# Kernel tuning notes

Hardware: AMD Instinct MI355X
Metric: run time of the kernel (lower is better)

Reference implementation:

```python
import jax, jax.numpy as jnp
import numpy as np

NBINS = 256  # tf.histogram_fixed_width(..., nbins=256)


def _colorspace():
    # tf.clip_by_value(tf.range(-1.0, 1.01, delta=1/127), -1, 1) -> 256 values
    cs = -1.0 + jnp.arange(NBINS, dtype=jnp.float32) / 127.0
    return jnp.clip(cs, -1.0, 1.0)


def _equalize_histogram(chan):
    # chan: (H, W) float32 in [-1, 1]
    h, w = chan.shape
    v = jnp.clip(chan.ravel(), -1.0, 1.0)
    idx = jnp.clip(((v + 1.0) * (NBINS / 2.0)).astype(jnp.int32), 0, NBINS - 1)
    hist = jnp.zeros(NBINS, jnp.int32).at[idx].add(1)
    cdf = jnp.cumsum(hist)
    cdf_min = jnp.min(cdf)
    pix_cnt = float(h * w)
    return (cdf - cdf_min).astype(jnp.float32) * 2.0 / (pix_cnt - 1.0) - 1.0


def _interpolate(dx, dy, x):
    # dx, dy: (K,) ; x: (N,) -> (N,) piecewise-linear interp via nearest-bin argmin
    delvals = jnp.abs(dx[None, :] - x[:, None])  # (N, K) big intermediate, as in TF
    ind1 = jnp.argmin(delvals, axis=1)
    ind0 = jnp.maximum(ind1 - 1, 0)
    x0, x1 = dx[ind0], dx[ind1]
    y0, y1 = dy[ind0], dy[ind1]
    denom = x1 - x0
    safe = jnp.where(denom == 0.0, 1.0, denom)  # guard flat-CDF degenerate bins
    interp = y0 + (y1 - y0) * (x - x0) / safe
    return jnp.where(x <= dx[0], dy[0], jnp.where(x >= dx[-1], dy[-1], interp))


def setup_inputs() -> dict:
    key = jax.random.key(0)
    k1, k2 = jax.random.split(key)
    H, W = 1024, 1024
    src = jax.random.uniform(k1, (H, W, 3), jnp.float32, minval=-1.0, maxval=1.0)
    tgt = jax.random.uniform(k2, (H, W, 3), jnp.float32, minval=-1.0, maxval=1.0)
    return {"src": src, "tgt": tgt}


def reference(src, tgt):
    h, w, _ = src.shape
    cs = _colorspace()
    res = []
    for i in range(3):
        s = src[:, :, i]
        t = tgt[:, :, i]
        cdfsrc = _equalize_histogram(s)
        cdftgt = _equalize_histogram(t)
        pxmap = _interpolate(cdftgt, cs, cdfsrc)      # (256,) color map
        mapped = _interpolate(cs, pxmap, s.ravel())   # (H*W,) per-pixel lookup
        res.append(mapped.reshape(h, w))
    return jnp.stack(res, axis=2)
```

## Files before the change

kernel.cpp:

```cpp
#include <hip/hip_runtime.h>

#define NBINS 256
#define SLOT (6 * NBINS)

__device__ __forceinline__ float csv(int i) {
    float c = -1.0f + (float)i / 127.0f;
    return fminf(fmaxf(c, -1.0f), 1.0f);
}

__device__ __forceinline__ int binof(float v) {
    v = fminf(fmaxf(v, -1.0f), 1.0f);
    int b = (int)((v + 1.0f) * 128.0f);
    return min(max(b, 0), NBINS - 1);
}

__global__ __launch_bounds__(256) void hm_hist(const float* __restrict__ src,
                                               const float* __restrict__ tgt,
                                               int ngroups, int n,
                                               int* __restrict__ partials) {
    __shared__ int lh[SLOT];
    for (int i = threadIdx.x; i < SLOT; i += blockDim.x) lh[i] = 0;
    __syncthreads();

    const float4* __restrict__ s4 = (const float4*)src;
    const float4* __restrict__ t4 = (const float4*)tgt;
    const int stride = gridDim.x * blockDim.x;
    for (int g = blockIdx.x * blockDim.x + threadIdx.x; g < ngroups; g += stride) {
        int b = g * 3;
        float4 s0 = s4[b], s1 = s4[b + 1], s2 = s4[b + 2];
        float4 t0 = t4[b], t1 = t4[b + 1], t2 = t4[b + 2];
        atomicAdd(&lh[0 * NBINS + binof(s0.x)], 1);
        atomicAdd(&lh[1 * NBINS + binof(s0.y)], 1);
        atomicAdd(&lh[2 * NBINS + binof(s0.z)], 1);
        atomicAdd(&lh[0 * NBINS + binof(s0.w)], 1);
        atomicAdd(&lh[1 * NBINS + binof(s1.x)], 1);
        atomicAdd(&lh[2 * NBINS + binof(s1.y)], 1);
        atomicAdd(&lh[0 * NBINS + binof(s1.z)], 1);
        atomicAdd(&lh[1 * NBINS + binof(s1.w)], 1);
        atomicAdd(&lh[2 * NBINS + binof(s2.x)], 1);
        atomicAdd(&lh[0 * NBINS + binof(s2.y)], 1);
        atomicAdd(&lh[1 * NBINS + binof(s2.z)], 1);
        atomicAdd(&lh[2 * NBINS + binof(s2.w)], 1);

        atomicAdd(&lh[3 * NBINS + binof(t0.x)], 1);
        atomicAdd(&lh[4 * NBINS + binof(t0.y)], 1);
        atomicAdd(&lh[5 * NBINS + binof(t0.z)], 1);
        atomicAdd(&lh[3 * NBINS + binof(t0.w)], 1);
        atomicAdd(&lh[4 * NBINS + binof(t1.x)], 1);
        atomicAdd(&lh[5 * NBINS + binof(t1.y)], 1);
        atomicAdd(&lh[3 * NBINS + binof(t1.z)], 1);
        atomicAdd(&lh[4 * NBINS + binof(t1.w)], 1);
        atomicAdd(&lh[5 * NBINS + binof(t2.x)], 1);
        atomicAdd(&lh[3 * NBINS + binof(t2.y)], 1);
        atomicAdd(&lh[4 * NBINS + binof(t2.z)], 1);
        atomicAdd(&lh[5 * NBINS + binof(t2.w)], 1);
    }
    if (blockIdx.x == 0) {
        int base = ngroups * 12;
        int rem = n - base;
        if ((int)threadIdx.x < rem) {
            int j = base + threadIdx.x;
            int c = j % 3;
            atomicAdd(&lh[c * NBINS + binof(src[j])], 1);
            atomicAdd(&lh[(3 + c) * NBINS + binof(tgt[j])], 1);
        }
    }
    __syncthreads();

    int* dst = partials + blockIdx.x * SLOT;
    for (int i = threadIdx.x; i < SLOT; i += blockDim.x) dst[i] = lh[i];
}

__global__ __launch_bounds__(1024) void hm_tables(const int* __restrict__ partials,
                                                  int nslots,
                                                  float pixcnt_m1,
                                                  float* __restrict__ pxmap) {
    const int c = blockIdx.x;
    const int t = threadIdx.x;
    const int grp = t >> 8;
    const int bin = t & 255;

    __shared__ int red[8][NBINS];
    __shared__ int ss[NBINS], st[NBINS];
    __shared__ float cdfs[NBINS], cdft[NBINS];

    int as = 0, at = 0;
    const int offS = c * NBINS + bin;
    const int offT = (3 + c) * NBINS + bin;
    #pragma unroll 8
    for (int b = grp; b < nslots; b += 4) {
        const int* p = partials + b * SLOT;
        as += p[offS];
        at += p[offT];
    }
    red[grp][bin] = as;
    red[4 + grp][bin] = at;
    __syncthreads();

    if (t < NBINS) {
        ss[t] = red[0][t] + red[1][t] + red[2][t] + red[3][t];
        st[t] = red[4][t] + red[5][t] + red[6][t] + red[7][t];
    }
    __syncthreads();

    for (int off = 1; off < NBINS; off <<= 1) {
        int a = 0, b = 0;
        if (t < NBINS && t >= off) { a = ss[t - off]; b = st[t - off]; }
        __syncthreads();
        if (t < NBINS && t >= off) { ss[t] += a; st[t] += b; }
        __syncthreads();
    }

    if (t < NBINS) {
        int mins = ss[0];
        int mint = st[0];
        cdfs[t] = (float)(ss[t] - mins) * 2.0f / pixcnt_m1 - 1.0f;
        cdft[t] = (float)(st[t] - mint) * 2.0f / pixcnt_m1 - 1.0f;
    }
    __syncthreads();

    if (t < NBINS) {
        float x = cdfs[t];
        int ind1 = 0;
        float best = fabsf(cdft[0] - x);
        for (int i = 1; i < NBINS; i++) {
            float d = fabsf(cdft[i] - x);
            if (d < best) { best = d; ind1 = i; }
        }
        int ind0 = max(ind1 - 1, 0);
        float x0 = cdft[ind0], x1 = cdft[ind1];
        float y0 = csv(ind0),  y1 = csv(ind1);
        float denom = x1 - x0;
        float safe = (denom == 0.0f) ? 1.0f : denom;
        float interp = y0 + (y1 - y0) * (x - x0) / safe;

        float r;
        if (x <= cdft[0])              r = csv(0);
        else if (x >= cdft[NBINS - 1]) r = csv(NBINS - 1);
        else                           r = interp;

        pxmap[c * NBINS + t] = r;
    }
}

__device__ __forceinline__ float map_one(float x, const float* __restrict__ y,
                                         const float* __restrict__ cs) {
    if (x <= -1.0f) return y[0];
    if (x >= 1.0f)  return y[NBINS - 1];
    float kf = (x + 1.0f) * 127.0f;
    int k = (int)(kf + 0.5f);
    int lo = max(k - 1, 0);
    int hi = min(k + 1, NBINS - 1);
    int ind1 = lo;
    float best = fabsf(cs[lo] - x);
    for (int j = lo + 1; j <= hi; j++) {
        float d = fabsf(cs[j] - x);
        if (d < best) { best = d; ind1 = j; }
    }
    int ind0 = max(ind1 - 1, 0);
    float x0 = cs[ind0], x1 = cs[ind1];
    float y0 = y[ind0],  y1 = y[ind1];
    float denom = x1 - x0;
    float safe = (denom == 0.0f) ? 1.0f : denom;
    return y0 + (y1 - y0) * (x - x0) / safe;
}

__global__ __launch_bounds__(256) void hm_map(const float* __restrict__ src,
                                              const float* __restrict__ pxmap,
                                              float* __restrict__ out,
                                              int ngroups, int n) {
    __shared__ float pm[3 * NBINS];
    __shared__ float cs[NBINS];
    for (int i = threadIdx.x; i < 3 * NBINS; i += blockDim.x) pm[i] = pxmap[i];
    for (int i = threadIdx.x; i < NBINS; i += blockDim.x) cs[i] = csv(i);
    __syncthreads();

    const float4* __restrict__ s4 = (const float4*)src;
    float4* __restrict__ o4 = (float4*)out;
    const int stride = gridDim.x * blockDim.x;
    for (int g = blockIdx.x * blockDim.x + threadIdx.x; g < ngroups; g += stride) {
        int b = g * 3;
        float4 s0 = s4[b], s1 = s4[b + 1], s2 = s4[b + 2];
        float4 r0, r1, r2;
        r0.x = map_one(s0.x, &pm[0 * NBINS], cs);
        r0.y = map_one(s0.y, &pm[1 * NBINS], cs);
        r0.z = map_one(s0.z, &pm[2 * NBINS], cs);
        r0.w = map_one(s0.w, &pm[0 * NBINS], cs);
        r1.x = map_one(s1.x, &pm[1 * NBINS], cs);
        r1.y = map_one(s1.y, &pm[2 * NBINS], cs);
        r1.z = map_one(s1.z, &pm[0 * NBINS], cs);
        r1.w = map_one(s1.w, &pm[1 * NBINS], cs);
        r2.x = map_one(s2.x, &pm[2 * NBINS], cs);
        r2.y = map_one(s2.y, &pm[0 * NBINS], cs);
        r2.z = map_one(s2.z, &pm[1 * NBINS], cs);
        r2.w = map_one(s2.w, &pm[2 * NBINS], cs);
        o4[b] = r0; o4[b + 1] = r1; o4[b + 2] = r2;
    }
    if (blockIdx.x == 0) {
        int base = ngroups * 12;
        int rem = n - base;
        if ((int)threadIdx.x < rem) {
            int j = base + threadIdx.x;
            int c = j % 3;
            out[j] = map_one(src[j], &pm[c * NBINS], cs);
        }
    }
}

extern "C" void kernel_launch(void* const* d_in, const int* in_sizes, int n_in,
                              void* d_out, int out_size, void* d_ws, size_t ws_size,
                              hipStream_t stream) {
    const float* src = (const float*)d_in[0];
    const float* tgt = (const float*)d_in[1];
    float* out = (float*)d_out;

    const int n = in_sizes[0];
    const int ngroups = n / 12;
    const int pixcnt = n / 3;

    float* pxmap    = (float*)d_ws;
    int*   partials = (int*)((char*)d_ws + 4096);

    const int slot_bytes = SLOT * (int)sizeof(int);
    int NB = 512;
    int need = (ngroups + 255) / 256;
    if (need < 1) need = 1;
    if (NB > need) NB = need;
    if (ws_size >= 4096 + (size_t)slot_bytes) {
        size_t avail = (ws_size - 4096) / slot_bytes;
        if (avail < (size_t)NB) NB = (int)avail;
    } else {
        NB = 1;
    }

    hm_hist<<<NB, 256, 0, stream>>>(src, tgt, ngroups, n, partials);

    hm_tables<<<3, 1024, 0, stream>>>(partials, NB, (float)pixcnt - 1.0f, pxmap);

    int mblocks = (ngroups + 255) / 256;
    if (mblocks > 1024) mblocks = 1024;
    if (mblocks < 1) mblocks = 1;
    hm_map<<<mblocks, 256, 0, stream>>>(src, pxmap, out, ngroups, n);
}
```

Measured before the change: 108.8 us.

## Fuse histogram reduction and CDF table build via last-block atomic merge

Merges the histogram and table kernels into one. Each block atomically adds its shared histogram into one of four global copies, and the last block to finish (found with a done counter) sums the copies, builds the CDFs and writes the pixel map. This removes a kernel launch and the per-block partials write and reread. In exchange it adds a memset, global atomics, and a serial tail in which a single block handles all three channels one after another. The grid size also drops from 512 to 256 blocks.

```diff
diff --git a/kernel.cpp b/kernel.cpp
--- a/kernel.cpp
+++ b/kernel.cpp
@@ -2,6 +2,7 @@
 
 #define NBINS 256
 #define SLOT (6 * NBINS)
+#define NCOPY 4
 
 __device__ __forceinline__ float csv(int i) {
     float c = -1.0f + (float)i / 127.0f;
@@ -14,18 +15,44 @@
     return min(max(b, 0), NBINS - 1);
 }
 
-__global__ __launch_bounds__(256) void hm_hist(const float* __restrict__ src,
-                                               const float* __restrict__ tgt,
-                                               int ngroups, int n,
-                                               int* __restrict__ partials) {
+__device__ __forceinline__ float map_one(float x, const float* __restrict__ y,
+                                         const float* __restrict__ cs) {
+    if (x <= -1.0f) return y[0];
+    if (x >= 1.0f)  return y[NBINS - 1];
+    float kf = (x + 1.0f) * 127.0f;
+    int k = (int)(kf + 0.5f);
+    int lo = max(k - 1, 0);
+    int hi = min(k + 1, NBINS - 1);
+    int ind1 = lo;
+    float best = fabsf(cs[lo] - x);
+    for (int j = lo + 1; j <= hi; j++) {
+        float d = fabsf(cs[j] - x);
+        if (d < best) { best = d; ind1 = j; }
+    }
+    int ind0 = max(ind1 - 1, 0);
+    float x0 = cs[ind0], x1 = cs[ind1];
+    float y0 = y[ind0],  y1 = y[ind1];
+    float denom = x1 - x0;
+    float safe = (denom == 0.0f) ? 1.0f : denom;
+    return y0 + (y1 - y0) * (x - x0) / safe;
+}
+
+__global__ __launch_bounds__(256) void hm_hist_tables(const float* __restrict__ src,
+                                                      const float* __restrict__ tgt,
+                                                      int ngroups, int n,
+                                                      float pixcnt_m1,
+                                                      int* __restrict__ ghist,
+                                                      unsigned int* __restrict__ done,
+                                                      float* __restrict__ pxmap) {
     __shared__ int lh[SLOT];
-    for (int i = threadIdx.x; i < SLOT; i += blockDim.x) lh[i] = 0;
+    const int t = threadIdx.x;
+    for (int i = t; i < SLOT; i += blockDim.x) lh[i] = 0;
     __syncthreads();
 
     const float4* __restrict__ s4 = (const float4*)src;
     const float4* __restrict__ t4 = (const float4*)tgt;
     const int stride = gridDim.x * blockDim.x;
-    for (int g = blockIdx.x * blockDim.x + threadIdx.x; g < ngroups; g += stride) {
+    for (int g = blockIdx.x * blockDim.x + t; g < ngroups; g += stride) {
         int b = g * 3;
         float4 s0 = s4[b], s1 = s4[b + 1], s2 = s4[b + 2];
         float4 t0 = t4[b], t1 = t4[b + 1], t2 = t4[b + 2];
@@ -58,8 +85,8 @@
     if (blockIdx.x == 0) {
         int base = ngroups * 12;
         int rem = n - base;
-        if ((int)threadIdx.x < rem) {
-            int j = base + threadIdx.x;
+        if (t < rem) {
+            int j = base + t;
             int c = j % 3;
             atomicAdd(&lh[c * NBINS + binof(src[j])], 1);
             atomicAdd(&lh[(3 + c) * NBINS + binof(tgt[j])], 1);
@@ -67,102 +94,77 @@
     }
     __syncthreads();
 
-    int* dst = partials + blockIdx.x * SLOT;
-    for (int i = threadIdx.x; i < SLOT; i += blockDim.x) dst[i] = lh[i];
-}
-
-__global__ __launch_bounds__(1024) void hm_tables(const int* __restrict__ partials,
-                                                  int nslots,
-                                                  float pixcnt_m1,
-                                                  float* __restrict__ pxmap) {
-    const int c = blockIdx.x;
-    const int t = threadIdx.x;
-    const int grp = t >> 8;
-    const int bin = t & 255;
-
-    __shared__ int red[8][NBINS];
+    {
+        int* gdst = ghist + (blockIdx.x & (NCOPY - 1)) * SLOT;
+        for (int i = t; i < SLOT; i += blockDim.x) {
+            int v = lh[i];
+            if (v) atomicAdd(&gdst[i], v);
+        }
+    }
+
+    __shared__ unsigned int is_last;
+    __threadfence();
+    __syncthreads();
+    if (t == 0) {
+        unsigned int prev = atomicAdd(done, 1u);
+        is_last = (prev == gridDim.x - 1) ? 1u : 0u;
+    }
+    __syncthreads();
+    if (!is_last) return;
+    __threadfence();
+
     __shared__ int ss[NBINS], st[NBINS];
     __shared__ float cdfs[NBINS], cdft[NBINS];
 
-    int as = 0, at = 0;
-    const int offS = c * NBINS + bin;
-    const int offT = (3 + c) * NBINS + bin;
-    #pragma unroll 8
-    for (int b = grp; b < nslots; b += 4) {
-        const int* p = partials + b * SLOT;
-        as += p[offS];
-        at += p[offT];
-    }
-    red[grp][bin] = as;
-    red[4 + grp][bin] = at;
-    __syncthreads();
-
-    if (t < NBINS) {
-        ss[t] = red[0][t] + red[1][t] + red[2][t] + red[3][t];
-        st[t] = red[4][t] + red[5][t] + red[6][t] + red[7][t];
-    }
-    __syncthreads();
-
-    for (int off = 1; off < NBINS; off <<= 1) {
-        int a = 0, b = 0;
-        if (t < NBINS && t >= off) { a = ss[t - off]; b = st[t - off]; }
+    for (int c = 0; c < 3; ++c) {
+        int a0 = 0, a1 = 0;
+        #pragma unroll
+        for (int k = 0; k < NCOPY; ++k) {
+            a0 += __hip_atomic_load(&ghist[k * SLOT + c * NBINS + t],
+                                    __ATOMIC_RELAXED, __HIP_MEMORY_SCOPE_AGENT);
+            a1 += __hip_atomic_load(&ghist[k * SLOT + (3 + c) * NBINS + t],
+                                    __ATOMIC_RELAXED, __HIP_MEMORY_SCOPE_AGENT);
+        }
+        ss[t] = a0;
+        st[t] = a1;
         __syncthreads();
-        if (t < NBINS && t >= off) { ss[t] += a; st[t] += b; }
+
+        for (int off = 1; off < NBINS; off <<= 1) {
+            int a = 0, b = 0;
+            if (t >= off) { a = ss[t - off]; b = st[t - off]; }
+            __syncthreads();
+            if (t >= off) { ss[t] += a; st[t] += b; }
+            __syncthreads();
+        }
+
+        cdfs[t] = (float)(ss[t] - ss[0]) * 2.0f / pixcnt_m1 - 1.0f;
+        cdft[t] = (float)(st[t] - st[0]) * 2.0f / pixcnt_m1 - 1.0f;
         __syncthreads();
-    }
-
-    if (t < NBINS) {
-        int mins = ss[0];
-        int mint = st[0];
-        cdfs[t] = (float)(ss[t] - mins) * 2.0f / pixcnt_m1 - 1.0f;
-        cdft[t] = (float)(st[t] - mint) * 2.0f / pixcnt_m1 - 1.0f;
-    }
-    __syncthreads();
-
-    if (t < NBINS) {
-        float x = cdfs[t];
-        int ind1 = 0;
-        float best = fabsf(cdft[0] - x);
-        for (int i = 1; i < NBINS; i++) {
-            float d = fabsf(cdft[i] - x);
-            if (d < best) { best = d; ind1 = i; }
-        }
-        int ind0 = max(ind1 - 1, 0);
-        float x0 = cdft[ind0], x1 = cdft[ind1];
-        float y0 = csv(ind0),  y1 = csv(ind1);
-        float denom = x1 - x0;
-        float safe = (denom == 0.0f) ? 1.0f : denom;
-        float interp = y0 + (y1 - y0) * (x - x0) / safe;
-
-        float r;
-        if (x <= cdft[0])              r = csv(0);
-        else if (x >= cdft[NBINS - 1]) r = csv(NBINS - 1);
-        else                           r = interp;
-
-        pxmap[c * NBINS + t] = r;
-    }
-}
-
-__device__ __forceinline__ float map_one(float x, const float* __restrict__ y,
-                                         const float* __restrict__ cs) {
-    if (x <= -1.0f) return y[0];
-    if (x >= 1.0f)  return y[NBINS - 1];
-    float kf = (x + 1.0f) * 127.0f;
-    int k = (int)(kf + 0.5f);
-    int lo = max(k - 1, 0);
-    int hi = min(k + 1, NBINS - 1);
-    int ind1 = lo;
-    float best = fabsf(cs[lo] - x);
-    for (int j = lo + 1; j <= hi; j++) {
-        float d = fabsf(cs[j] - x);
-        if (d < best) { best = d; ind1 = j; }
-    }
-    int ind0 = max(ind1 - 1, 0);
-    float x0 = cs[ind0], x1 = cs[ind1];
-    float y0 = y[ind0],  y1 = y[ind1];
-    float denom = x1 - x0;
-    float safe = (denom == 0.0f) ? 1.0f : denom;
-    return y0 + (y1 - y0) * (x - x0) / safe;
+
+        {
+            float x = cdfs[t];
+            int ind1 = 0;
+            float best = fabsf(cdft[0] - x);
+            for (int i = 1; i < NBINS; i++) {
+                float d = fabsf(cdft[i] - x);
+                if (d < best) { best = d; ind1 = i; }
+            }
+            int ind0 = max(ind1 - 1, 0);
+            float x0 = cdft[ind0], x1 = cdft[ind1];
+            float y0 = csv(ind0),  y1 = csv(ind1);
+            float denom = x1 - x0;
+            float safe = (denom == 0.0f) ? 1.0f : denom;
+            float interp = y0 + (y1 - y0) * (x - x0) / safe;
+
+            float r;
+            if (x <= cdft[0])              r = csv(0);
+            else if (x >= cdft[NBINS - 1]) r = csv(NBINS - 1);
+            else                           r = interp;
+
+            pxmap[c * NBINS + t] = r;
+        }
+        __syncthreads();
+    }
 }
 
 __global__ __launch_bounds__(256) void hm_map(const float* __restrict__ src,
@@ -217,25 +219,22 @@
     const int n = in_sizes[0];
     const int ngroups = n / 12;
     const int pixcnt = n / 3;
-
-    float* pxmap    = (float*)d_ws;
-    int*   partials = (int*)((char*)d_ws + 4096);
-
-    const int slot_bytes = SLOT * (int)sizeof(int);
-    int NB = 512;
+    float pixm1 = (float)pixcnt - 1.0f;
+
+    float*        pxmap = (float*)d_ws;
+    int*          ghist = (int*)((char*)d_ws + 4096);
+    unsigned int* done  = (unsigned int*)((char*)d_ws + 4096 + NCOPY * SLOT * sizeof(int));
+
+    hipMemsetAsync((char*)d_ws + 4096, 0,
+                   NCOPY * SLOT * sizeof(int) + sizeof(unsigned int), stream);
+
+    int NB = 256;
     int need = (ngroups + 255) / 256;
     if (need < 1) need = 1;
     if (NB > need) NB = need;
-    if (ws_size >= 4096 + (size_t)slot_bytes) {
-        size_t avail = (ws_size - 4096) / slot_bytes;
-        if (avail < (size_t)NB) NB = (int)avail;
-    } else {
-        NB = 1;
-    }
-
-    hm_hist<<<NB, 256, 0, stream>>>(src, tgt, ngroups, n, partials);
-
-    hm_tables<<<3, 1024, 0, stream>>>(partials, NB, (float)pixcnt - 1.0f, pxmap);
+
+    hm_hist_tables<<<NB, 256, 0, stream>>>(src, tgt, ngroups, n, pixm1,
+                                           ghist, done, pxmap);
 
     int mblocks = (ngroups + 255) / 256;
     if (mblocks > 1024) mblocks = 1024;
```

New measurement: 122.3 us. 1.12x slower.
